# Optimization experiments

Measured on AMD Instinct MI355X. Metric: run time of the kernel, lower is better.

## Reference

```python
import jax, jax.numpy as jnp
import numpy as np

B, N, C = 32, 512, 256          # batch, proposals per scene, pooled feature dim
K = 16                          # knn neighbors
NN = B * N                      # total nodes = 16384
E = NN * K                      # total edges = 262144
L0_IN = 2 * C + 7               # EdgeConv layer-0 input (edge embedding appended)
EPS = 1e-5


def _xavier(key, fan_in, fan_out):
    s = float(np.sqrt(6.0 / (fan_in + fan_out)))
    return jax.random.uniform(key, (fan_in, fan_out), jnp.float32, -s, s)


def setup_inputs() -> dict:
    key = jax.random.key(0)
    ks = jax.random.split(key, 12)
    inp = {}
    inp["pooled_features"] = jax.random.normal(ks[0], (B, N, C), jnp.float32)
    inp["rois"] = jax.random.normal(ks[1], (B, N, 7), jnp.float32)
    inp["edge_src"] = jax.random.randint(ks[2], (E,), 0, NN)
    inp["edge_dst"] = jax.random.randint(ks[3], (E,), 0, NN)
    # global-info MLP: Linear(C+7 -> C) + BatchNorm(C) + ReLU
    inp["Wg"] = _xavier(ks[4], C + 7, C)
    inp["bg"] = jnp.zeros((C,), jnp.float32)
    inp["gg"] = jnp.ones((C,), jnp.float32)
    inp["betag"] = jnp.zeros((C,), jnp.float32)
    # EdgeConv 0: Linear(2C+7 -> C); EdgeConv 1,2: Linear(2C -> C)
    inp["W0"] = _xavier(ks[5], L0_IN, C)
    inp["b0"] = jnp.zeros((C,), jnp.float32)
    inp["g0"] = jnp.ones((C,), jnp.float32)
    inp["beta0"] = jnp.zeros((C,), jnp.float32)
    inp["W1"] = _xavier(ks[6], 2 * C, C)
    inp["b1"] = jnp.zeros((C,), jnp.float32)
    inp["g1"] = jnp.ones((C,), jnp.float32)
    inp["beta1"] = jnp.zeros((C,), jnp.float32)
    inp["W2"] = _xavier(ks[7], 2 * C, C)
    inp["b2"] = jnp.zeros((C,), jnp.float32)
    inp["g2"] = jnp.ones((C,), jnp.float32)
    inp["beta2"] = jnp.zeros((C,), jnp.float32)
    return inp


def _bn_relu(h, gamma, beta):
    # training-mode BatchNorm over the row (node/edge) dimension
    mu = jnp.mean(h, axis=0)
    var = jnp.mean(jnp.square(h - mu), axis=0)
    return jax.nn.relu((h - mu) * jax.lax.rsqrt(var + EPS) * gamma + beta)


def _edge_conv(x, src, dst, edge_attr, W, b, gamma, beta):
    x_j = x[src]          # source-node features  [E, D]
    x_i = x[dst]          # target-node features  [E, D]
    parts = [x_j - x_i, x_i]
    if edge_attr is not None:
        parts.append(edge_attr)
    m = jnp.concatenate(parts, axis=-1)          # [E, in_dim]
    h = _bn_relu(m @ W + b, gamma, beta)         # [E, C]
    out = jax.ops.segment_max(h, dst, num_segments=NN)  # scatter-max per target node
    return jnp.where(jnp.isneginf(out), 0.0, out)        # empty segments -> 0


def reference(pooled_features, rois, edge_src, edge_dst,
              Wg, bg, gg, betag,
              W0, b0, g0, beta0,
              W1, b1, g1, beta1,
              W2, b2, g2, beta2):
    boxes = rois.reshape(NN, 7)
    pf = pooled_features.reshape(NN, C)
    # global information MLP (CONCATENATED): cat(pooled, boxes) -> Linear+BN+ReLU
    x0 = _bn_relu(jnp.concatenate([pf, boxes], axis=-1) @ Wg + bg, gg, betag)
    # edge embedding: box delta from source to target
    edge_attr = boxes[edge_src] - boxes[edge_dst]
    x1 = _edge_conv(x0, edge_src, edge_dst, edge_attr, W0, b0, g0, beta0)
    x2 = _edge_conv(x1, edge_src, edge_dst, None, W1, b1, g1, beta1)
    x3 = _edge_conv(x2, edge_src, edge_dst, None, W2, b2, g2, beta2)
    return jnp.concatenate([x0, x1, x2, x3], axis=-1)  # related_features [NN, 4C]
```

## Files before the change

kernel.cpp:

```cpp
#include <hip/hip_runtime.h>
#include <hip/hip_bf16.h>
#include <hip/hip_fp16.h>
#include <math.h>
#include <stdint.h>


constexpr int NNODE = 16384;
constexpr int NEDGE = 262144;
constexpr int CD    = 256;
constexpr float EPSB = 1e-5f;

typedef __attribute__((ext_vector_type(8))) short bf16x8;
typedef __attribute__((ext_vector_type(8))) unsigned short u16x8;
typedef __attribute__((ext_vector_type(4))) float f32x4;
typedef __attribute__((ext_vector_type(4))) _Float16 h16x4;
typedef __attribute__((ext_vector_type(8))) _Float16 h16x8;
typedef __attribute__((ext_vector_type(2))) _Float16 h16x2;

__device__ inline unsigned short bf_hi_rne(float f) {
  unsigned int u = __float_as_uint(f);
  u += 0x7fffu + ((u >> 16) & 1u);
  return (unsigned short)(u >> 16);
}

__device__ __forceinline__ void gload16(const void* g, void* l) {
  __builtin_amdgcn_global_load_lds(
      (__attribute__((address_space(1))) void*)(void*)g,
      (__attribute__((address_space(3))) void*)l, 16, 0, 0);
}

__global__ void build_wt(const float* __restrict__ W, const float* __restrict__ b,
                         unsigned short* __restrict__ Wth, int has_box) {
  int k = threadIdx.x;
  int n = blockIdx.x;
  if (k >= 288) return;
  float v = 0.0f;
  if (n < 256) {
    if (k < 256)      v = W[k * 256 + n];
    else if (k < 263) v = has_box ? W[(512 + (k - 256)) * 256 + n] : 0.0f;
  } else {
    int n2 = n - 256;
    if (k < 256)      v = W[(256 + k) * 256 + n2] - W[k * 256 + n2];
    else if (k < 263) v = has_box ? -W[(512 + (k - 256)) * 256 + n2] : 0.0f;
    else if (k == 263) v = b[n2];
  }
  Wth[n * 288 + k] = bf_hi_rne(v);
}

__global__ void build_wtg(const float* __restrict__ Wg, const float* __restrict__ bg,
                          unsigned short* __restrict__ Wth) {
  int k = threadIdx.x;
  int n = blockIdx.x;
  if (k >= 288) return;
  float v = 0.0f;
  if (k < 263)       v = Wg[k * 256 + n];
  else if (k == 263) v = bg[n];
  Wth[n * 288 + k] = bf_hi_rne(v);
}

__global__ void build_boxf16(const float* __restrict__ rois,
                             unsigned short* __restrict__ hi) {
  int n = blockIdx.x * 256 + threadIdx.x;
  u16x8 h8 = (u16x8)0;
#pragma unroll
  for (int j = 0; j < 8; j++) {
    float v = (j < 7) ? rois[n * 7 + j] : 1.0f;
    h8[j] = bf_hi_rne(v);
  }
  *(u16x8*)(hi + (size_t)n * 32) = h8;
  u16x8 z = (u16x8)0;
#pragma unroll
  for (int c = 1; c < 4; c++) *(u16x8*)(hi + (size_t)n * 32 + c * 8) = z;
}

__global__ void convert_split(const float* __restrict__ src,
                              unsigned short* __restrict__ hi) {
  size_t i0 = ((size_t)blockIdx.x * 256 + threadIdx.x) * 8;
  float4 a = *(const float4*)(src + i0);
  float4 b = *(const float4*)(src + i0 + 4);
  float v[8] = {a.x, a.y, a.z, a.w, b.x, b.y, b.z, b.w};
  u16x8 h8;
#pragma unroll
  for (int j = 0; j < 8; j++) h8[j] = bf_hi_rne(v[j]);
  *(u16x8*)(hi + i0) = h8;
}

__global__ void hist_kernel(const int* __restrict__ dst, int* __restrict__ counts) {
  int e = blockIdx.x * 256 + threadIdx.x;
  atomicAdd(&counts[dst[e]], 1);
}

__global__ __launch_bounds__(1024) void scan_kernel(const int* __restrict__ counts,
                                                    int* __restrict__ offsets,
                                                    int* __restrict__ cursor) {
  __shared__ int ssum[1024];
  int t = threadIdx.x;
  int base = t * 16;
  int loc[16];
  int s = 0;
#pragma unroll
  for (int i = 0; i < 16; i++) { loc[i] = s; s += counts[base + i]; }
  ssum[t] = s;
  __syncthreads();
  for (int off = 1; off < 1024; off <<= 1) {
    int v = (t >= off) ? ssum[t - off] : 0;
    __syncthreads();
    ssum[t] += v;
    __syncthreads();
  }
  int excl = (t > 0) ? ssum[t - 1] : 0;
#pragma unroll
  for (int i = 0; i < 16; i++) {
    int o = excl + loc[i];
    offsets[base + i] = o;
    cursor[base + i]  = o;
  }
  if (t == 1023) offsets[NNODE] = excl + s;
}

__global__ void scatter_kernel(const int* __restrict__ src, const int* __restrict__ dst,
                               int* __restrict__ cursor, int* __restrict__ csr_src) {
  int e = blockIdx.x * 256 + threadIdx.x;
  int p = atomicAdd(&cursor[dst[e]], 1);
  csr_src[p] = src[e];
}

__global__ __launch_bounds__(256) void gemm_mfma(
    const unsigned short* __restrict__ Ah,
    const unsigned short* __restrict__ bxh,
    const unsigned short* __restrict__ Wth,
    float* __restrict__ out, int Nw, int half_out) {
  __shared__ alignas(16) char lds[2 * 8192];
  const int tid  = threadIdx.x;
  const int lane = tid & 63;
  const int wave = tid >> 6;
  const int wm = wave >> 1, wn = wave & 1;
  const int m0 = blockIdx.x * 128;
  const int n0 = blockIdx.y * 128;
  const int srow = tid >> 2;
  const int sc8  = (tid & 3) * 8;

  f32x4 acc[4][4];
#pragma unroll
  for (int i = 0; i < 4; i++)
#pragma unroll
    for (int j = 0; j < 4; j++) acc[i][j] = (f32x4)0.0f;

  const int kblk = lane >> 4;
  for (int kt = 0; kt < 9; kt++) {
    if (kt) __syncthreads();
#pragma unroll
    for (int p = 0; p < 2; p++) {
      int row = p * 64 + srow;
      const unsigned short* ga =
          (kt < 8) ? Ah + (size_t)(m0 + row) * 256 + kt * 32 + sc8
                   : bxh + (size_t)(m0 + row) * 32 + sc8;
      gload16(ga, lds + p * 4096 + tid * 16);
      gload16(Wth + (size_t)(n0 + row) * 288 + kt * 32 + sc8,
              lds + 8192 + p * 4096 + tid * 16);
    }
    __syncthreads();

    bf16x8 ah[4];
#pragma unroll
    for (int i = 0; i < 4; i++) {
      int fm = wm * 64 + i * 16 + (lane & 15);
      ah[i] = *(const bf16x8*)(lds + fm * 64 + 16 * kblk);
    }
#pragma unroll
    for (int j = 0; j < 4; j++) {
      int fn = wn * 64 + j * 16 + (lane & 15);
      bf16x8 bh = *(const bf16x8*)(lds + 8192 + fn * 64 + 16 * kblk);
#pragma unroll
      for (int i = 0; i < 4; i++)
        acc[i][j] = __builtin_amdgcn_mfma_f32_16x16x32_bf16(bh, ah[i], acc[i][j], 0, 0, 0);
    }
  }
#pragma unroll
  for (int i = 0; i < 4; i++) {
    int m = m0 + wm * 64 + i * 16 + (lane & 15);
#pragma unroll
    for (int j = 0; j < 4; j++) {
      int n = n0 + wn * 64 + j * 16 + (lane >> 4) * 4;
      if (half_out) {
        h16x4 o;
        o[0] = (_Float16)acc[i][j].x; o[1] = (_Float16)acc[i][j].y;
        o[2] = (_Float16)acc[i][j].z; o[3] = (_Float16)acc[i][j].w;
        *(h16x4*)((_Float16*)out + (size_t)m * Nw + n) = o;
      } else {
        *(f32x4*)(out + (size_t)m * Nw + n) = acc[i][j];
      }
    }
  }
}

__global__ __launch_bounds__(512) void edge_pass(
    const _Float16* __restrict__ PQ,
    const int* __restrict__ offsets, const int* __restrict__ csr_src,
    float* __restrict__ M, float* __restrict__ psum, float* __restrict__ psq) {
  __shared__ float red[2][8][256];
  const int tid = threadIdx.x;
  const int wave = tid >> 6, lane = tid & 63;
  const int h = lane >> 5, li = lane & 31;
  const int c8 = li * 8;
  float sum[8] = {}, sq[8] = {};

  const int d = blockIdx.x * 8 + wave;
  const int beg = offsets[d], end = offsets[d + 1];
  const bool any = beg < end;

  if (any) {
    h16x8 qv = *(const h16x8*)(PQ + (size_t)d * 512 + 256 + c8);
    h16x2 q2[4], mx2[4];
    _Float16 NINF = (_Float16)(-INFINITY);
#pragma unroll
    for (int jj = 0; jj < 4; jj++) {
      q2[jj][0] = qv[2 * jj]; q2[jj][1] = qv[2 * jj + 1];
      mx2[jj][0] = NINF;      mx2[jj][1] = NINF;
    }

#define LOADIDX(I, E)                                                     \
    _Pragma("unroll") for (int i = 0; i < 4; i++) {                       \
      int ei = (E) + 2 * i + h;                                           \
      I[i] = csr_src[ei < end ? ei : end - 1];           \
    }
#define GATHER(P, I)                                                      \
    _Pragma("unroll") for (int i = 0; i < 4; i++)                         \
      P[i] = *(const h16x8*)(PQ + (size_t)I[i] * 512 + c8);
#define PROC(P, E)                                                        \
    {                                                                     \
      const int nl = end - (E);                                           \
      if (nl >= 8) {                                                      \
        _Pragma("unroll") for (int i = 0; i < 4; i++)                     \
          _Pragma("unroll") for (int jj = 0; jj < 4; jj++) {              \
            h16x2 pp; pp[0] = P[i][2 * jj]; pp[1] = P[i][2 * jj + 1];     \
            h16x2 hh = pp + q2[jj];                     \
            mx2[jj] = __builtin_elementwise_max(mx2[jj], hh);             \
            float h0 = (float)hh[0], h1 = (float)hh[1];                   \
            sum[2 * jj] += h0; sum[2 * jj + 1] += h1;                     \
            sq[2 * jj] = fmaf(h0, h0, sq[2 * jj]);                        \
            sq[2 * jj + 1] = fmaf(h1, h1, sq[2 * jj + 1]);                \
          }                                                               \
      } else {                                                            \
        _Pragma("unroll") for (int i = 0; i < 4; i++) {                   \
          const bool live = (2 * i + h) < nl;                             \
          _Pragma("unroll") for (int jj = 0; jj < 4; jj++) {              \
            h16x2 pp; pp[0] = P[i][2 * jj]; pp[1] = P[i][2 * jj + 1];     \
            h16x2 hh = pp + q2[jj];                                       \
            mx2[jj] = __builtin_elementwise_max(mx2[jj], hh);             \
            float h0 = (float)hh[0], h1 = (float)hh[1];                   \
            float z0 = live ? h0 : 0.f, z1 = live ? h1 : 0.f;             \
            sum[2 * jj] += z0; sum[2 * jj + 1] += z1;                     \
            sq[2 * jj] = fmaf(z0, z0, sq[2 * jj]);                        \
            sq[2 * jj + 1] = fmaf(z1, z1, sq[2 * jj + 1]);                \
          }                                                               \
        }                                                                 \
      }                                                                   \
    }

    int iA[4], iB[4];
    h16x8 pA[4], pB[4];
    LOADIDX(iA, beg);
    GATHER(pA, iA);
    if (beg + 8 < end) { LOADIDX(iB, beg + 8); GATHER(pB, iB); }
    int e = beg;
    while (true) {
      PROC(pA, e);
      if (e + 16 < end) { LOADIDX(iA, e + 16); GATHER(pA, iA); }
      e += 8;
      if (e >= end) break;
      PROC(pB, e);
      if (e + 16 < end) { LOADIDX(iB, e + 16); GATHER(pB, iB); }
      e += 8;
      if (e >= end) break;
    }
#undef LOADIDX
#undef GATHER
#undef PROC

    float mxf[8];
#pragma unroll
    for (int jj = 0; jj < 4; jj++) {
      mxf[2 * jj]     = (float)mx2[jj][0];
      mxf[2 * jj + 1] = (float)mx2[jj][1];
    }
#pragma unroll
    for (int j = 0; j < 8; j++)
      mxf[j] = fmaxf(mxf[j], __shfl_xor(mxf[j], 32));
    float4 o = (h == 0) ? make_float4(mxf[0], mxf[1], mxf[2], mxf[3])
                        : make_float4(mxf[4], mxf[5], mxf[6], mxf[7]);
    *(float4*)(M + (size_t)d * 256 + c8 + h * 4) = o;
  }

#pragma unroll
  for (int j = 0; j < 8; j++) {
    sum[j] += __shfl_xor(sum[j], 32);
    sq[j]  += __shfl_xor(sq[j], 32);
  }
  if (h == 0) {
    *(float4*)&red[0][wave][c8]     = make_float4(sum[0], sum[1], sum[2], sum[3]);
    *(float4*)&red[0][wave][c8 + 4] = make_float4(sum[4], sum[5], sum[6], sum[7]);
    *(float4*)&red[1][wave][c8]     = make_float4(sq[0], sq[1], sq[2], sq[3]);
    *(float4*)&red[1][wave][c8 + 4] = make_float4(sq[4], sq[5], sq[6], sq[7]);
  }
  __syncthreads();
  if (tid < 256) {
    float ts = 0.f, tq = 0.f;
#pragma unroll
    for (int w = 0; w < 8; w++) { ts += red[0][w][tid]; tq += red[1][w][tid]; }
    atomicAdd(&psum[tid], ts);
    atomicAdd(&psq[tid], tq);
  }
}

__global__ void stats_dense(const float* __restrict__ H,
                            float* __restrict__ psum, float* __restrict__ psq) {
  int c  = threadIdx.x;
  int r0 = blockIdx.x * 16;
  float sum = 0.f, sq = 0.f;
  for (int r = r0; r < r0 + 16; r++) {
    float h = H[r * CD + c];
    sum += h;
    sq  += h * h;
  }
  atomicAdd(&psum[c], sum);
  atomicAdd(&psq[c], sq);
}

__global__ void finalize_stats(const float* __restrict__ psum, const float* __restrict__ psq,
                               float invcount, float* __restrict__ mu, float* __restrict__ rstd) {
  int c = threadIdx.x;
  float m = psum[c] * invcount;
  float v = psq[c] * invcount - m * m;
  v = fmaxf(v, 0.0f);
  mu[c]   = m;
  rstd[c] = 1.0f / sqrtf(v + EPSB);
}

__global__ void normalize_write(const float* __restrict__ H, const int* __restrict__ counts,
                                const float* __restrict__ mu, const float* __restrict__ rstd,
                                const float* __restrict__ gamma, const float* __restrict__ beta,
                                float* __restrict__ out, int col0,
                                unsigned short* __restrict__ xh) {
  int c  = threadIdx.x;
  int n0 = blockIdx.x * 8;
  float mc = mu[c], rc = rstd[c], gc = gamma[c], bc = beta[c];
  for (int n = n0; n < n0 + 8; n++) {
    float v = 0.0f;
    if (!counts || counts[n] != 0) {
      float h = H[n * CD + c];
      v = fmaxf((h - mc) * rc * gc + bc, 0.0f);
    }
    out[n * 1024 + col0 + c] = v;
    if (xh) xh[(size_t)n * 256 + c] = bf_hi_rne(v);
  }
}

extern "C" void kernel_launch(void* const* d_in, const int* in_sizes, int n_in,
                              void* d_out, int out_size, void* d_ws, size_t ws_size,
                              hipStream_t stream) {
  const float* pf    = (const float*)d_in[0];
  const float* rois  = (const float*)d_in[1];
  const int*   esrc  = (const int*)d_in[2];
  const int*   edst  = (const int*)d_in[3];
  const float* Wg    = (const float*)d_in[4];
  const float* bg    = (const float*)d_in[5];
  const float* gg    = (const float*)d_in[6];
  const float* betag = (const float*)d_in[7];
  const float* Wl[3]  = {(const float*)d_in[8],  (const float*)d_in[12], (const float*)d_in[16]};
  const float* bl[3]  = {(const float*)d_in[9],  (const float*)d_in[13], (const float*)d_in[17]};
  const float* gl[3]  = {(const float*)d_in[10], (const float*)d_in[14], (const float*)d_in[18]};
  const float* bel[3] = {(const float*)d_in[11], (const float*)d_in[15], (const float*)d_in[19]};
  float* out = (float*)d_out;

  float* ws    = (float*)d_ws;
  _Float16* PQ = (_Float16*)ws;
  float* Mbuf  = ws + (size_t)NNODE * 256;
  float* psum  = Mbuf + (size_t)NNODE * CD;
  float* psq   = psum + CD;
  float* mu    = psq + CD;
  float* rstd  = mu + CD;
  unsigned short* Ah  = (unsigned short*)(rstd + CD);
  unsigned short* bxh = Ah + (size_t)NNODE * 256;
  unsigned short* wt  = bxh + (size_t)NNODE * 32;
  unsigned short* wtg = wt + 3 * 512 * 288;
  int* counts  = (int*)(wtg + 256 * 288);
  int* offsets = counts + NNODE;
  int* cursor  = offsets + NNODE + 1;
  int* csr     = cursor + NNODE;

  hipMemsetAsync(counts, 0, NNODE * sizeof(int), stream);
  build_boxf16<<<NNODE / 256, 256, 0, stream>>>(rois, bxh);
  convert_split<<<NNODE * CD / (256 * 8), 256, 0, stream>>>(pf, Ah);
  build_wtg<<<256, 320, 0, stream>>>(Wg, bg, wtg);
  for (int l = 0; l < 3; l++)
    build_wt<<<512, 320, 0, stream>>>(Wl[l], bl[l], wt + l * 512 * 288, l == 0 ? 1 : 0);
  hist_kernel<<<NEDGE / 256, 256, 0, stream>>>(edst, counts);
  scan_kernel<<<1, 1024, 0, stream>>>(counts, offsets, cursor);
  scatter_kernel<<<NEDGE / 256, 256, 0, stream>>>(esrc, edst, cursor, csr);

  hipMemsetAsync(psum, 0, 2 * CD * sizeof(float), stream);
  {
    dim3 g(NNODE / 128, 2);
    gemm_mfma<<<g, 256, 0, stream>>>(Ah, bxh, wtg, Mbuf, 256, 0);
  }
  stats_dense<<<NNODE / 16, 256, 0, stream>>>(Mbuf, psum, psq);
  finalize_stats<<<1, 256, 0, stream>>>(psum, psq, 1.0f / NNODE, mu, rstd);
  normalize_write<<<NNODE / 8, 256, 0, stream>>>(Mbuf, nullptr, mu, rstd, gg, betag,
                                                 out, 0, Ah);

  for (int l = 0; l < 3; l++) {
    dim3 g(NNODE / 128, 4);
    gemm_mfma<<<g, 256, 0, stream>>>(Ah, bxh, wt + l * 512 * 288, (float*)PQ, 512, 1);
    hipMemsetAsync(psum, 0, 2 * CD * sizeof(float), stream);
    edge_pass<<<NNODE / 8, 512, 0, stream>>>(PQ, offsets, csr, Mbuf, psum, psq);
    finalize_stats<<<1, 256, 0, stream>>>(psum, psq, 1.0f / NEDGE, mu, rstd);
    normalize_write<<<NNODE / 8, 256, 0, stream>>>(Mbuf, counts, mu, rstd, gl[l], bel[l],
                                                   out, (l + 1) * CD,
                                                   l < 2 ? Ah : nullptr);
  }
}
```

Baseline: 460.4 us.

## Decompose edge BN statistics into per-node dense terms and drop finalize kernels

Edge pre-activations are h = P[src] + Q[dst], so their sum and sum of squares are rebuilt algebraically. Per-node terms weighted by in- and out-degree go into a new dense_terms kernel, and the edge pass only accumulates the gathered P sums for the cross term. The per-edge max is taken over P alone with Q added once afterwards, which removes the per-edge fp16 add and most of the per-edge square accumulation. Mean and rstd are computed inside normalize_write, which removes the finalize_stats launches and the per-layer memsets; the cost is an extra out-degree histogram and a saturating fp16 store to keep the expanded sums finite.

```diff
diff --git a/kernel.cpp b/kernel.cpp
--- a/kernel.cpp
+++ b/kernel.cpp
@@ -27,6 +27,10 @@
   __builtin_amdgcn_global_load_lds(
       (__attribute__((address_space(1))) void*)(void*)g,
       (__attribute__((address_space(3))) void*)l, 16, 0, 0);
+}
+
+__device__ __forceinline__ _Float16 to_h16_sat(float f) {
+  return (_Float16)fminf(fmaxf(f, -65504.0f), 65504.0f);
 }
 
 __global__ void build_wt(const float* __restrict__ W, const float* __restrict__ b,
@@ -85,9 +89,9 @@
   *(u16x8*)(hi + i0) = h8;
 }
 
-__global__ void hist_kernel(const int* __restrict__ dst, int* __restrict__ counts) {
+__global__ void hist_kernel(const int* __restrict__ idx, int* __restrict__ counts) {
   int e = blockIdx.x * 256 + threadIdx.x;
-  atomicAdd(&counts[dst[e]], 1);
+  atomicAdd(&counts[idx[e]], 1);
 }
 
 __global__ __launch_bounds__(1024) void scan_kernel(const int* __restrict__ counts,
@@ -184,8 +188,8 @@
       int n = n0 + wn * 64 + j * 16 + (lane >> 4) * 4;
       if (half_out) {
         h16x4 o;
-        o[0] = (_Float16)acc[i][j].x; o[1] = (_Float16)acc[i][j].y;
-        o[2] = (_Float16)acc[i][j].z; o[3] = (_Float16)acc[i][j].w;
+        o[0] = to_h16_sat(acc[i][j].x); o[1] = to_h16_sat(acc[i][j].y);
+        o[2] = to_h16_sat(acc[i][j].z); o[3] = to_h16_sat(acc[i][j].w);
         *(h16x4*)((_Float16*)out + (size_t)m * Nw + n) = o;
       } else {
         *(f32x4*)(out + (size_t)m * Nw + n) = acc[i][j];
@@ -194,6 +198,24 @@
   }
 }
 
+__global__ void dense_terms(const _Float16* __restrict__ PQ,
+                            const int* __restrict__ indeg, const int* __restrict__ outdeg,
+                            float* __restrict__ psum, float* __restrict__ psq) {
+  int c  = threadIdx.x;
+  int n0 = blockIdx.x * 8;
+  float s = 0.f, s2 = 0.f;
+  for (int n = n0; n < n0 + 8; n++) {
+    float oc = (float)outdeg[n], ic = (float)indeg[n];
+    float p = (float)PQ[(size_t)n * 512 + c];
+    float q = (float)PQ[(size_t)n * 512 + 256 + c];
+    s  += ic * q;
+    s2 += oc * p * p + ic * q * q;
+  }
+  atomicAdd(&psum[c], s);
+  atomicAdd(&psq[c], s2);
+}
+
+constexpr int EPB = 8;
 __global__ __launch_bounds__(512) void edge_pass(
     const _Float16* __restrict__ PQ,
     const int* __restrict__ offsets, const int* __restrict__ csr_src,
@@ -203,21 +225,18 @@
   const int wave = tid >> 6, lane = tid & 63;
   const int h = lane >> 5, li = lane & 31;
   const int c8 = li * 8;
-  float sum[8] = {}, sq[8] = {};
-
-  const int d = blockIdx.x * 8 + wave;
+  float S[8] = {};
+  float cs[8] = {}, cq[8] = {};
+
+  const int d = blockIdx.x * EPB + wave;
   const int beg = offsets[d], end = offsets[d + 1];
-  const bool any = beg < end;
-
-  if (any) {
+
+  if (beg < end) {
     h16x8 qv = *(const h16x8*)(PQ + (size_t)d * 512 + 256 + c8);
-    h16x2 q2[4], mx2[4];
+    h16x2 mx2[4];
     _Float16 NINF = (_Float16)(-INFINITY);
 #pragma unroll
-    for (int jj = 0; jj < 4; jj++) {
-      q2[jj][0] = qv[2 * jj]; q2[jj][1] = qv[2 * jj + 1];
-      mx2[jj][0] = NINF;      mx2[jj][1] = NINF;
-    }
+    for (int jj = 0; jj < 4; jj++) { mx2[jj][0] = NINF; mx2[jj][1] = NINF; }
 
 #define LOADIDX(I, E)                                                     \
     _Pragma("unroll") for (int i = 0; i < 4; i++) {                       \
@@ -231,29 +250,23 @@
     {                                                                     \
       const int nl = end - (E);                                           \
       if (nl >= 8) {                                                      \
-        _Pragma("unroll") for (int i = 0; i < 4; i++)                     \
+        _Pragma("unroll") for (int i = 0; i < 4; i++) {                   \
           _Pragma("unroll") for (int jj = 0; jj < 4; jj++) {              \
             h16x2 pp; pp[0] = P[i][2 * jj]; pp[1] = P[i][2 * jj + 1];     \
-            h16x2 hh = pp + q2[jj];                     \
-            mx2[jj] = __builtin_elementwise_max(mx2[jj], hh);             \
-            float h0 = (float)hh[0], h1 = (float)hh[1];                   \
-            sum[2 * jj] += h0; sum[2 * jj + 1] += h1;                     \
-            sq[2 * jj] = fmaf(h0, h0, sq[2 * jj]);                        \
-            sq[2 * jj + 1] = fmaf(h1, h1, sq[2 * jj + 1]);                \
+            mx2[jj] = __builtin_elementwise_max(mx2[jj], pp);             \
           }                                                               \
+          _Pragma("unroll") for (int j = 0; j < 8; j++)                   \
+            S[j] += (float)P[i][j];                                       \
+        }                                                                 \
       } else {                                                            \
         _Pragma("unroll") for (int i = 0; i < 4; i++) {                   \
           const bool live = (2 * i + h) < nl;                             \
           _Pragma("unroll") for (int jj = 0; jj < 4; jj++) {              \
             h16x2 pp; pp[0] = P[i][2 * jj]; pp[1] = P[i][2 * jj + 1];     \
-            h16x2 hh = pp + q2[jj];                                       \
-            mx2[jj] = __builtin_elementwise_max(mx2[jj], hh);             \
-            float h0 = (float)hh[0], h1 = (float)hh[1];                   \
-            float z0 = live ? h0 : 0.f, z1 = live ? h1 : 0.f;             \
-            sum[2 * jj] += z0; sum[2 * jj + 1] += z1;                     \
-            sq[2 * jj] = fmaf(z0, z0, sq[2 * jj]);                        \
-            sq[2 * jj + 1] = fmaf(z1, z1, sq[2 * jj + 1]);                \
+            mx2[jj] = __builtin_elementwise_max(mx2[jj], pp);             \
           }                                                               \
+          _Pragma("unroll") for (int j = 0; j < 8; j++)                   \
+            S[j] += live ? (float)P[i][j] : 0.f;                          \
         }                                                                 \
       }                                                                   \
     }
@@ -278,30 +291,34 @@
 #undef GATHER
 #undef PROC
 
-    float mxf[8];
+    float mxf[8], q8[8];
 #pragma unroll
     for (int jj = 0; jj < 4; jj++) {
       mxf[2 * jj]     = (float)mx2[jj][0];
       mxf[2 * jj + 1] = (float)mx2[jj][1];
     }
 #pragma unroll
-    for (int j = 0; j < 8; j++)
+    for (int j = 0; j < 8; j++) {
+      q8[j] = (float)qv[j];
       mxf[j] = fmaxf(mxf[j], __shfl_xor(mxf[j], 32));
-    float4 o = (h == 0) ? make_float4(mxf[0], mxf[1], mxf[2], mxf[3])
-                        : make_float4(mxf[4], mxf[5], mxf[6], mxf[7]);
+      S[j]  += __shfl_xor(S[j], 32);
+    }
+    float4 o = (h == 0)
+      ? make_float4(mxf[0] + q8[0], mxf[1] + q8[1], mxf[2] + q8[2], mxf[3] + q8[3])
+      : make_float4(mxf[4] + q8[4], mxf[5] + q8[5], mxf[6] + q8[6], mxf[7] + q8[7]);
     *(float4*)(M + (size_t)d * 256 + c8 + h * 4) = o;
-  }
-
-#pragma unroll
-  for (int j = 0; j < 8; j++) {
-    sum[j] += __shfl_xor(sum[j], 32);
-    sq[j]  += __shfl_xor(sq[j], 32);
-  }
+#pragma unroll
+    for (int j = 0; j < 8; j++) {
+      cs[j] = S[j];
+      cq[j] = 2.0f * q8[j] * S[j];
+    }
+  }
+
   if (h == 0) {
-    *(float4*)&red[0][wave][c8]     = make_float4(sum[0], sum[1], sum[2], sum[3]);
-    *(float4*)&red[0][wave][c8 + 4] = make_float4(sum[4], sum[5], sum[6], sum[7]);
-    *(float4*)&red[1][wave][c8]     = make_float4(sq[0], sq[1], sq[2], sq[3]);
-    *(float4*)&red[1][wave][c8 + 4] = make_float4(sq[4], sq[5], sq[6], sq[7]);
+    *(float4*)&red[0][wave][c8]     = make_float4(cs[0], cs[1], cs[2], cs[3]);
+    *(float4*)&red[0][wave][c8 + 4] = make_float4(cs[4], cs[5], cs[6], cs[7]);
+    *(float4*)&red[1][wave][c8]     = make_float4(cq[0], cq[1], cq[2], cq[3]);
+    *(float4*)&red[1][wave][c8 + 4] = make_float4(cq[4], cq[5], cq[6], cq[7]);
   }
   __syncthreads();
   if (tid < 256) {
@@ -327,32 +344,25 @@
   atomicAdd(&psq[c], sq);
 }
 
-__global__ void finalize_stats(const float* __restrict__ psum, const float* __restrict__ psq,
-                               float invcount, float* __restrict__ mu, float* __restrict__ rstd) {
-  int c = threadIdx.x;
-  float m = psum[c] * invcount;
-  float v = psq[c] * invcount - m * m;
-  v = fmaxf(v, 0.0f);
-  mu[c]   = m;
-  rstd[c] = 1.0f / sqrtf(v + EPSB);
-}
-
 __global__ void normalize_write(const float* __restrict__ H, const int* __restrict__ counts,
-                                const float* __restrict__ mu, const float* __restrict__ rstd,
+                                const float* __restrict__ psum, const float* __restrict__ psq,
+                                float invcount,
                                 const float* __restrict__ gamma, const float* __restrict__ beta,
                                 float* __restrict__ out, int col0,
                                 unsigned short* __restrict__ xh) {
   int c  = threadIdx.x;
   int n0 = blockIdx.x * 8;
-  float mc = mu[c], rc = rstd[c], gc = gamma[c], bc = beta[c];
+  float m = psum[c] * invcount;
+  float v = fmaxf(psq[c] * invcount - m * m, 0.0f);
+  float rc = (1.0f / sqrtf(v + EPSB)) * gamma[c];
+  float bc = beta[c];
   for (int n = n0; n < n0 + 8; n++) {
-    float v = 0.0f;
+    float val = 0.0f;
     if (!counts || counts[n] != 0) {
-      float h = H[n * CD + c];
-      v = fmaxf((h - mc) * rc * gc + bc, 0.0f);
-    }
-    out[n * 1024 + col0 + c] = v;
-    if (xh) xh[(size_t)n * 256 + c] = bf_hi_rne(v);
+      val = fmaxf((H[n * CD + c] - m) * rc + bc, 0.0f);
+    }
+    out[n * 1024 + col0 + c] = val;
+    if (xh) xh[(size_t)n * 256 + c] = bf_hi_rne(val);
   }
 }
 
@@ -376,46 +386,45 @@
   float* ws    = (float*)d_ws;
   _Float16* PQ = (_Float16*)ws;
   float* Mbuf  = ws + (size_t)NNODE * 256;
-  float* psum  = Mbuf + (size_t)NNODE * CD;
-  float* psq   = psum + CD;
-  float* mu    = psq + CD;
-  float* rstd  = mu + CD;
-  unsigned short* Ah  = (unsigned short*)(rstd + CD);
+  unsigned short* Ah  = (unsigned short*)(Mbuf + (size_t)NNODE * CD);
   unsigned short* bxh = Ah + (size_t)NNODE * 256;
   unsigned short* wt  = bxh + (size_t)NNODE * 32;
   unsigned short* wtg = wt + 3 * 512 * 288;
   int* counts  = (int*)(wtg + 256 * 288);
-  int* offsets = counts + NNODE;
+  int* outdeg  = counts + NNODE;
+  float* stats = (float*)(outdeg + NNODE);
+  int* offsets = (int*)(stats + 4 * 512);
   int* cursor  = offsets + NNODE + 1;
   int* csr     = cursor + NNODE;
 
-  hipMemsetAsync(counts, 0, NNODE * sizeof(int), stream);
+  hipMemsetAsync(counts, 0, 2 * NNODE * sizeof(int) + 4 * 512 * sizeof(float), stream);
   build_boxf16<<<NNODE / 256, 256, 0, stream>>>(rois, bxh);
   convert_split<<<NNODE * CD / (256 * 8), 256, 0, stream>>>(pf, Ah);
   build_wtg<<<256, 320, 0, stream>>>(Wg, bg, wtg);
   for (int l = 0; l < 3; l++)
     build_wt<<<512, 320, 0, stream>>>(Wl[l], bl[l], wt + l * 512 * 288, l == 0 ? 1 : 0);
   hist_kernel<<<NEDGE / 256, 256, 0, stream>>>(edst, counts);
+  hist_kernel<<<NEDGE / 256, 256, 0, stream>>>(esrc, outdeg);
   scan_kernel<<<1, 1024, 0, stream>>>(counts, offsets, cursor);
   scatter_kernel<<<NEDGE / 256, 256, 0, stream>>>(esrc, edst, cursor, csr);
 
-  hipMemsetAsync(psum, 0, 2 * CD * sizeof(float), stream);
   {
     dim3 g(NNODE / 128, 2);
     gemm_mfma<<<g, 256, 0, stream>>>(Ah, bxh, wtg, Mbuf, 256, 0);
   }
-  stats_dense<<<NNODE / 16, 256, 0, stream>>>(Mbuf, psum, psq);
-  finalize_stats<<<1, 256, 0, stream>>>(psum, psq, 1.0f / NNODE, mu, rstd);
-  normalize_write<<<NNODE / 8, 256, 0, stream>>>(Mbuf, nullptr, mu, rstd, gg, betag,
-                                                 out, 0, Ah);
+  stats_dense<<<NNODE / 16, 256, 0, stream>>>(Mbuf, stats, stats + 256);
+  normalize_write<<<NNODE / 8, 256, 0, stream>>>(Mbuf, nullptr, stats, stats + 256,
+                                                 1.0f / NNODE, gg, betag, out, 0, Ah);
 
   for (int l = 0; l < 3; l++) {
+    float* ps = stats + (l + 1) * 512;
+    float* pq = ps + 256;
     dim3 g(NNODE / 128, 4);
     gemm_mfma<<<g, 256, 0, stream>>>(Ah, bxh, wt + l * 512 * 288, (float*)PQ, 512, 1);
-    hipMemsetAsync(psum, 0, 2 * CD * sizeof(float), stream);
-    edge_pass<<<NNODE / 8, 512, 0, stream>>>(PQ, offsets, csr, Mbuf, psum, psq);
-    finalize_stats<<<1, 256, 0, stream>>>(psum, psq, 1.0f / NEDGE, mu, rstd);
-    normalize_write<<<NNODE / 8, 256, 0, stream>>>(Mbuf, counts, mu, rstd, gl[l], bel[l],
+    dense_terms<<<NNODE / 8, 256, 0, stream>>>(PQ, counts, outdeg, ps, pq);
+    edge_pass<<<NNODE / EPB, 512, 0, stream>>>(PQ, offsets, csr, Mbuf, ps, pq);
+    normalize_write<<<NNODE / 8, 256, 0, stream>>>(Mbuf, counts, ps, pq,
+                                                   1.0f / NEDGE, gl[l], bel[l],
                                                    out, (l + 1) * CD,
                                                    l < 2 ? Ah : nullptr);
   }
```

Measured after the change: 610.5 us. 1.33x slower.
